# Performance work log

Measured on AMD Instinct MI355X. Metric: run time of the kernel, lower is better.

The kernel has to match this reference:

```python
import jax, jax.numpy as jnp
import numpy as np
from jax import lax

STRIDE = 2
PADDING = 2
KSIZE = 5


def _maxpool3d(y, k):
    # valid max pool with kernel=stride=k over the 3 spatial dims of NCDHW
    return lax.reduce_window(
        y, -jnp.inf, lax.max,
        window_dimensions=(1, 1, k, k, k),
        window_strides=(1, 1, k, k, k),
        padding='VALID')


def setup_inputs() -> dict:
    key = jax.random.key(0)
    k1, k2, k3 = jax.random.split(key, 3)
    x = jax.random.normal(k1, (16, 32, 16, 32, 32), dtype=jnp.float32)
    # torch ConvTranspose3d weight layout: (in_ch, out_ch, kD, kH, kW)
    weight = jax.random.normal(k2, (32, 64, KSIZE, KSIZE, KSIZE), dtype=jnp.float32) * 0.05
    bias = jax.random.normal(k3, (64,), dtype=jnp.float32) * 0.05
    return {"x": x, "weight": weight, "bias": bias}


def reference(x, weight, bias):
    # Fused ConvTranspose3d + sum over output channels.
    # sum_c convT(x, W)[:, c] == convT(x, W.sum(out_ch)) + bias.sum(), so we
    # pre-reduce the weight over the out-channel axis (axis=1) -- same math,
    # and it never materializes the (N, out_ch, D', H', W') intermediate,
    # exactly like the fused CUDA kernel.
    w_sum = weight.sum(axis=1)  # (in_ch, kD, kH, kW)
    # transposed conv == conv with lhs_dilation=stride, pad k-1-p, flipped kernel
    wk = w_sum[None, :, ::-1, ::-1, ::-1]  # (1, in_ch, kD, kH, kW), OIDHW
    pad = KSIZE - 1 - PADDING
    y = lax.conv_general_dilated(
        x, wk,
        window_strides=(1, 1, 1),
        padding=[(pad, pad)] * 3,
        lhs_dilation=(STRIDE, STRIDE, STRIDE),
        dimension_numbers=('NCDHW', 'OIDHW', 'NCDHW'))  # (N,1,31,63,63)
    y = y + bias.sum()
    # MaxPool3d(kernel=2) then MaxPool3d(kernel=3) on the single-channel map
    y = _maxpool3d(y, 2)  # (N,1,15,31,31)
    y = _maxpool3d(y, 3)  # (N,1,5,10,10)
    return y
```

## Files before the change

kernel.cpp:

```cpp
#include <hip/hip_runtime.h>


typedef short v8s __attribute__((ext_vector_type(8)));
typedef float v4f __attribute__((ext_vector_type(4)));
typedef unsigned short ushort_t;

#define CHSTR 16384
#define NSTRIDE (32*CHSTR)
#define Y_N 108000
#define Y_TOT (16*Y_N)
#define XSTR 24

#define XT_US 10653696u
#define XTN   665856u
#define PLANE_US 36992u
#define ROW_US 1088u
#define BT_BYTE_OFF 21307392u
#define WSF_BYTE_OFF 21335040u
#define NEED_MFMA (21335040u + 4097u*4u)

static __device__ __forceinline__ ushort_t f2bf(float f) {
  unsigned u = __builtin_bit_cast(unsigned, f);
  unsigned r = (u + 0x7FFFu + ((u >> 16) & 1u)) >> 16;
  return (ushort_t)r;
}

__global__ __launch_bounds__(256) void transpose_x(const float* __restrict__ x,
                                                   const float* __restrict__ w,
                                                   const float* __restrict__ bias,
                                                   ushort_t* __restrict__ xT,
                                                   ushort_t* __restrict__ Btab,
                                                   float* __restrict__ wsf) {
  int blk = blockIdx.x;
  int t = threadIdx.x;

  if (blk >= 1088) {
    int abc = blk - 1088;
    int a = abc / 9, b = (abc / 3) % 3, c = abc % 3;
    int half = t & 3;
    int l = t >> 2;
    int tt = l & 15, g = l >> 4;
    float v0 = 0.f, v1 = 0.f;
    if (tt < 8) {
      int td = tt & 1, th = (tt >> 1) & 1, tw = tt >> 2;
      int kd = td + 2 * a, kh = th + 2 * b, kw = tw + 2 * c;
      if (kd < 5 && kh < 5 && kw < 5) {
        int off = kd * 25 + kh * 5 + kw;
        const float* wp0 = w + (size_t)(8 * g + 2 * half) * 64 * 125 + off;
        const float* wp1 = wp0 + 64 * 125;
        float s0 = 0.f, s1 = 0.f;
#pragma unroll
        for (int oc = 0; oc < 64; ++oc) { s0 += wp0[oc * 125]; s1 += wp1[oc * 125]; }
        v0 = s0; v1 = s1;
      }
    }
    ((unsigned*)Btab)[(abc * 64 + l) * 4 + half] = (unsigned)f2bf(v0) | ((unsigned)f2bf(v1) << 16);
    if (abc == 0 && t == 0) {
      float bsum = 0.f;
      for (int o = 0; o < 64; ++o) bsum += bias[o];
      wsf[4096] = bsum;
    }
    return;
  }

  int hq = blk & 3;
  int dpad = (blk >> 2) % 17;
  int n = blk / 68;
  int h0 = 8 * hq;
  ushort_t* plane = xT + (size_t)(n * 18 + dpad) * PLANE_US;
  int d = dpad - 1;

  if (d < 0) {
    for (int r = 0; r < 8; ++r) {
      char* row = (char*)(plane + (size_t)(h0 + r) * ROW_US);
      for (int s = t; s < 136; s += 256)
        *(uint4*)(row + s * 16) = make_uint4(0, 0, 0, 0);
    }
    return;
  }

  __shared__ float lb[2][32 * 33];
  const float* xb = x + ((size_t)n * 32 * 16 + d) * 1024;
  int ic = t >> 3, wq = t & 7;

  {
    int h = h0 - 1;
    if (h >= 0) {
      float4 v = *(const float4*)&xb[(size_t)ic * 16384 + h * 32 + wq * 4];
      float* L = lb[0] + ic * 33 + wq * 4;
      L[0] = v.x; L[1] = v.y; L[2] = v.z; L[3] = v.w;
    }
  }
  int pp = 0;
  for (int i = 0; i < 8; ++i) {
    __syncthreads();
    if (i + 1 < 8) {
      int h = h0 + i;
      if (h <= 31) {
        float4 v = *(const float4*)&xb[(size_t)ic * 16384 + h * 32 + wq * 4];
        float* L = lb[pp ^ 1] + ic * 33 + wq * 4;
        L[0] = v.x; L[1] = v.y; L[2] = v.z; L[3] = v.w;
      }
    }
    int h = h0 + i - 1;
    ushort_t* row = plane + (size_t)(h0 + i) * ROW_US;
    bool hv = (h >= 0 && h <= 31);
    for (int s = t; s < 136; s += 256) {
      int wslot = s >> 2, q4 = s & 3;
      ushort_t o[8];
#pragma unroll
      for (int j = 0; j < 8; ++j) o[j] = 0;
      if (wslot >= 1 && wslot <= 32 && hv) {
        int w2 = wslot - 1;
        const float* L = lb[pp];
#pragma unroll
        for (int j = 0; j < 8; ++j) o[j] = f2bf(L[(8 * q4 + j) * 33 + w2]);
      }
      uint4 pk;
      pk.x = (unsigned)o[0] | ((unsigned)o[1] << 16);
      pk.y = (unsigned)o[2] | ((unsigned)o[3] << 16);
      pk.z = (unsigned)o[4] | ((unsigned)o[5] << 16);
      pk.w = (unsigned)o[6] | ((unsigned)o[7] << 16);
      *(uint4*)(row + wslot * 32 + q4 * 8) = pk;
    }
    pp ^= 1;
  }
}

__global__ __launch_bounds__(576, 7) void conv_mfma6(const ushort_t* __restrict__ xT,
                                                     const ushort_t* __restrict__ Btab,
                                                     const float* __restrict__ wsf,
                                                     float* __restrict__ out) {
  __shared__ __align__(16) char smem[35328];
  ushort_t* As0 = (ushort_t*)smem;
  ushort_t* As1 = (ushort_t*)(smem + 17408);
  float* ytile  = (float*)smem;
  float* red    = (float*)(smem + 34816);

  int blk = blockIdx.x;
  int OH2 = blk % 5, OD = (blk / 5) % 5, n = blk / 25;
  int t = threadIdx.x;
  int wv = t >> 6, l = t & 63;
  int mdl = wv / 3, mhp = wv % 3;
  int tt = l & 15, g = l >> 4;

  const ushort_t* xn = xT + (size_t)n * XTN;
  const ushort_t* slab0 = xn + ((size_t)(3 * OD) * 34 + 6 * OH2) * ROW_US;

  {
    uint4 v0 = *(const uint4*)(slab0 + (size_t)t * 8);
    uint4 v1;
    if (t < 512) v1 = *(const uint4*)(slab0 + (size_t)(t + 576) * 8);
    *(uint4*)&As0[t * 8] = v0;
    if (t < 512) *(uint4*)&As0[(t + 576) * 8] = v1;
  }
  __syncthreads();

  v4f acc[2][2];
#pragma unroll
  for (int m2 = 0; m2 < 2; ++m2)
#pragma unroll
    for (int wh = 0; wh < 2; ++wh) acc[m2][wh] = (v4f){0.f, 0.f, 0.f, 0.f};

  int lane_base = (2 * mhp) * ROW_US + tt * 32 + g * 8;

  for (int p = 0; p < 5; ++p) {
    uint4 v0, v1;
    if (p < 4) {
      const ushort_t* slab = slab0 + (size_t)(p + 1) * PLANE_US;
      v0 = *(const uint4*)(slab + (size_t)t * 8);
      if (t < 512) v1 = *(const uint4*)(slab + (size_t)(t + 576) * 8);
    }

    int a = mdl + 2 - p;
    if (0 <= a && a <= 2) {
      const ushort_t* Ab = (p & 1) ? As1 : As0;
      const ushort_t* Bg = Btab + ((size_t)(a * 9) * 64 + l) * 8;
#pragma unroll
      for (int c = 0; c < 3; ++c) {
        v8s bv0 = *(const v8s*)(Bg + (0 * 3 + c) * 512);
        v8s bv1 = *(const v8s*)(Bg + (1 * 3 + c) * 512);
        v8s bv2 = *(const v8s*)(Bg + (2 * 3 + c) * 512);
#pragma unroll
        for (int wh = 0; wh < 2; ++wh) {
          const ushort_t* ap = Ab + lane_base + (2 - c + 16 * wh) * 32;
          v8s a0 = *(const v8s*)(ap);
          v8s a1 = *(const v8s*)(ap + 1 * ROW_US);
          v8s a2 = *(const v8s*)(ap + 2 * ROW_US);
          v8s a3 = *(const v8s*)(ap + 3 * ROW_US);
          acc[0][wh] = __builtin_amdgcn_mfma_f32_16x16x32_bf16(a0, bv2, acc[0][wh], 0, 0, 0);
          acc[0][wh] = __builtin_amdgcn_mfma_f32_16x16x32_bf16(a1, bv1, acc[0][wh], 0, 0, 0);
          acc[0][wh] = __builtin_amdgcn_mfma_f32_16x16x32_bf16(a2, bv0, acc[0][wh], 0, 0, 0);
          acc[1][wh] = __builtin_amdgcn_mfma_f32_16x16x32_bf16(a1, bv2, acc[1][wh], 0, 0, 0);
          acc[1][wh] = __builtin_amdgcn_mfma_f32_16x16x32_bf16(a2, bv1, acc[1][wh], 0, 0, 0);
          acc[1][wh] = __builtin_amdgcn_mfma_f32_16x16x32_bf16(a3, bv0, acc[1][wh], 0, 0, 0);
        }
      }
    }

    if (p < 4) {
      ushort_t* dst = (p & 1) ? As0 : As1;
      *(uint4*)&dst[t * 8] = v0;
      if (t < 512) *(uint4*)&dst[(t + 576) * 8] = v1;
      __syncthreads();
    }
  }

  __syncthreads();
  if (tt < 8) {
    int td = tt & 1, th = (tt >> 1) & 1, tw = tt >> 2;
    int odl = 2 * mdl + td;
#pragma unroll
    for (int m2 = 0; m2 < 2; ++m2) {
      int ohl = 2 * (2 * mhp + m2) + th;
      float* yrow = &ytile[(odl * 12 + ohl) * 64];
#pragma unroll
      for (int wh = 0; wh < 2; ++wh)
#pragma unroll
        for (int i = 0; i < 4; ++i)
          yrow[2 * (16 * wh + 4 * g + i) + tw] = acc[m2][wh][i];
    }
  }
  __syncthreads();

  if (t < 120) {
    int OW = t % 10, p_oh = (t / 10) & 1, odl = t / 20;
    float m = -3.4e38f;
    for (int oh = 0; oh < 6; ++oh)
#pragma unroll
      for (int j = 0; j < 6; ++j)
        m = fmaxf(m, ytile[(odl * 12 + 6 * p_oh + oh) * 64 + 6 * OW + j]);
    red[t] = m;
  }
  __syncthreads();
  if (t < 20) {
    int OW = t % 10, p_oh = t / 10;
    float m = red[p_oh * 10 + OW];
#pragma unroll
    for (int odl = 1; odl < 6; ++odl) m = fmaxf(m, red[odl * 20 + p_oh * 10 + OW]);
    out[((n * 5 + OD) * 10 + (2 * OH2 + p_oh)) * 10 + OW] = m + wsf[4096];
  }
}

__global__ __launch_bounds__(128) void prep2(const float* __restrict__ w,
                                             const float* __restrict__ bias,
                                             float* __restrict__ ws, int woff) {
  int i = blockIdx.x, t = threadIdx.x;
  if (t < 125) {
    const float* wp = w + (size_t)i * 64 * 125 + t;
    float v = 0.f;
#pragma unroll
    for (int o = 0; o < 64; ++o) v += wp[o * 125];
    ws[woff + i * 128 + t] = v;
  }
  if (i == 0 && t == 126) {
    float b = 0.f;
    for (int o = 0; o < 64; ++o) b += bias[o];
    ws[woff + 4096] = b;
  }
}

__global__ __launch_bounds__(256, 4) void conv_stage1(const float* __restrict__ x,
                                                      const float* __restrict__ ws,
                                                      float* part, int woff) {
  __shared__ __align__(16) float xs[170 * XSTR];
  int blk = blockIdx.x;
  int s0 = blk % 320;
  int wq = s0 & 1, hq = (s0 >> 1) & 1, dc = (s0 >> 2) % 5, n = s0 / 20;
  int t = threadIdx.x;
  int mw = t % 15, lmh = t / 15;
  int id_base = 3 * dc - 1, ih_base = 15 * hq - 1;
  int iwb = wq ? 12 : -4;
  int cb = mw + (wq ? 2 : 3);
  const float* xn = x + (size_t)n * NSTRIDE;
  const float* wsw = ws + woff;
  float acc[3][2][2][2] = {{{{0.f}}}};
  for (int phs = 0; phs < 16; ++phs) {
    for (int s = t; s < 1700; s += 256) {
      int c2 = s % 10, row = s / 10;
      int bh = row % 17, q = row / 17;
      int ad = q % 5, lic = q / 5;
      int id = id_base + ad, ih = ih_base + bh, iw = iwb + 2 * c2;
      float2 v = make_float2(0.f, 0.f);
      if ((id | ih | iw) >= 0)
        v = *(const float2*)&xn[(size_t)(phs * 2 + lic) * CHSTR + (id * 32 + ih) * 32 + iw];
      *(float2*)&xs[row * XSTR + 2 * c2] = v;
    }
    __syncthreads();
    if (t < 225) {
#pragma unroll
      for (int lic = 0; lic < 2; ++lic) {
        const float* wc = wsw + (size_t)(phs * 2 + lic) * 128;
        const float* xc = &xs[(lic * 85 + lmh) * XSTR + cb];
        float xv[5][3][3];
#pragma unroll
        for (int a = 0; a < 5; ++a)
#pragma unroll
          for (int b = 0; b < 3; ++b) {
            const float* xr = xc + (a * 17 + b) * XSTR;
            xv[a][b][0] = xr[0]; xv[a][b][1] = xr[1]; xv[a][b][2] = xr[2];
          }
#pragma unroll
        for (int kd = 0; kd < 5; ++kd) {
          constexpr int DT[5] = {0, 1, 0, 1, 0};
          constexpr int AOFF[5] = {2, 2, 1, 1, 0};
          const int dt = DT[kd], aoff = AOFF[kd];
          float wvv[25];
#pragma unroll
          for (int j = 0; j < 25; ++j) wvv[j] = wc[kd * 25 + j];
#pragma unroll
          for (int kh = 0; kh < 5; ++kh) {
            constexpr int HT[5] = {0, 1, 0, 1, 0};
            constexpr int BOFF[5] = {2, 2, 1, 1, 0};
            const int ht = HT[kh], boff = BOFF[kh];
#pragma unroll
            for (int m = 0; m < 3; ++m) {
              const float x0 = xv[m + aoff][boff][0];
              const float x1 = xv[m + aoff][boff][1];
              const float x2 = xv[m + aoff][boff][2];
              acc[m][dt][ht][0] += x0 * wvv[kh * 5 + 4];
              acc[m][dt][ht][0] += x1 * wvv[kh * 5 + 2];
              acc[m][dt][ht][0] += x2 * wvv[kh * 5 + 0];
              acc[m][dt][ht][1] += x1 * wvv[kh * 5 + 3];
              acc[m][dt][ht][1] += x2 * wvv[kh * 5 + 1];
            }
          }
        }
      }
    }
    __syncthreads();
  }
  if (t < 225) {
    float* pb = part + (size_t)n * Y_N;
#pragma unroll
    for (int m = 0; m < 3; ++m)
#pragma unroll
      for (int dt = 0; dt < 2; ++dt)
#pragma unroll
        for (int ht = 0; ht < 2; ++ht) {
          int od_g = 6 * dc + 2 * m + dt;
          int oh_g = 30 * hq + 2 * lmh + ht;
          int ow_g = 30 * wq + 2 * mw;
          *(float2*)&pb[(od_g * 60 + oh_g) * 60 + ow_g] =
              make_float2(acc[m][dt][ht][0], acc[m][dt][ht][1]);
        }
  }
}

__global__ __launch_bounds__(256) void pool_stage2(const float* __restrict__ part,
                                                   const float* __restrict__ ws,
                                                   float* __restrict__ out, int woff) {
  __shared__ __align__(16) float buf[2160];
  __shared__ float red[240];
  int blk = blockIdx.x;
  int hc = blk % 10, dc = (blk / 10) % 5, n = blk / 50;
  int t = threadIdx.x;
  const float* pb = part + (size_t)n * Y_N;
  for (int s = t; s < 540; s += 256) {
    int row = s / 15, c4 = s % 15;
    int od = row / 6, oh = row % 6;
    size_t idx = (size_t)((6 * dc + od) * 60 + (6 * hc + oh)) * 60 + 4 * c4;
    *(float4*)&buf[row * 60 + 4 * c4] = *(const float4*)&pb[idx];
  }
  __syncthreads();
  if (t < 240) {
    int wc = t / 24, sub = t % 24;
    float m = -3.4e38f;
#pragma unroll
    for (int k = 0; k < 9; ++k) {
      int e = sub + 24 * k;
      int od = e / 36, r = e % 36;
      int oh = r / 6, ow0 = r % 6;
      m = fmaxf(m, buf[(od * 6 + oh) * 60 + 6 * wc + ow0]);
    }
    red[t] = m;
  }
  __syncthreads();
  if (t < 10) {
    float mm = -3.4e38f;
#pragma unroll
    for (int s2 = 0; s2 < 24; ++s2) mm = fmaxf(mm, red[t * 24 + s2]);
    out[((n * 5 + dc) * 10 + hc) * 10 + t] = mm + ws[woff + 4096];
  }
}

extern "C" void kernel_launch(void* const* d_in, const int* in_sizes, int n_in,
                              void* d_out, int out_size, void* d_ws, size_t ws_size,
                              hipStream_t stream) {
  const float* x    = (const float*)d_in[0];
  const float* w    = (const float*)d_in[1];
  const float* bias = (const float*)d_in[2];
  float* outp = (float*)d_out;

  if (ws_size >= (size_t)NEED_MFMA) {
    ushort_t* xT = (ushort_t*)d_ws;
    ushort_t* Bt = (ushort_t*)((char*)d_ws + BT_BYTE_OFF);
    float* wsf   = (float*)((char*)d_ws + WSF_BYTE_OFF);
    transpose_x<<<1088 + 27, 256, 0, stream>>>(x, w, bias, xT, Bt, wsf);
    conv_mfma6<<<400, 576, 0, stream>>>(xT, Bt, wsf, outp);
    return;
  }

  float* ws = (float*)d_ws;
  const size_t need1 = ((size_t)1 * Y_TOT + 4097) * 4;
  if (ws_size >= need1) {
    int woff = Y_TOT;
    prep2<<<32, 128, 0, stream>>>(w, bias, ws, woff);
    conv_stage1<<<320, 256, 0, stream>>>(x, ws, ws, woff);
    pool_stage2<<<800, 256, 0, stream>>>(ws, ws, outp, woff);
  }
}
```

Baseline: 36.05 us.

## Fuse x transpose and bf16 conversion into the MFMA conv kernel

Removes the separate transpose_x pass that wrote a padded bf16 channels-last copy of x to workspace. The conv kernel now reads fp32 x directly, converts it to bf16 and packs it into LDS, masking the halo rows and planes. It also remaps block indices so batch items spread across XCDs. This saves a full global round trip for x at the cost of strided, less coalesced loads in the conv kernel and a lower occupancy hint (5 instead of 7).

```diff
diff --git a/kernel.cpp b/kernel.cpp
--- a/kernel.cpp
+++ b/kernel.cpp
@@ -10,127 +10,56 @@
 #define Y_N 108000
 #define Y_TOT (16*Y_N)
 #define XSTR 24
-
-#define XT_US 10653696u
-#define XTN   665856u
-#define PLANE_US 36992u
-#define ROW_US 1088u
-#define BT_BYTE_OFF 21307392u
-#define WSF_BYTE_OFF 21335040u
-#define NEED_MFMA (21335040u + 4097u*4u)
+#define ROW_US 1088
+
+#define WSF_BYTE_OFF 27648u
+#define NEED_FUSED (27648u + 4097u*4u)
 
 static __device__ __forceinline__ ushort_t f2bf(float f) {
   unsigned u = __builtin_bit_cast(unsigned, f);
   unsigned r = (u + 0x7FFFu + ((u >> 16) & 1u)) >> 16;
   return (ushort_t)r;
 }
-
-__global__ __launch_bounds__(256) void transpose_x(const float* __restrict__ x,
-                                                   const float* __restrict__ w,
-                                                   const float* __restrict__ bias,
-                                                   ushort_t* __restrict__ xT,
-                                                   ushort_t* __restrict__ Btab,
-                                                   float* __restrict__ wsf) {
-  int blk = blockIdx.x;
+static __device__ __forceinline__ unsigned pk2(float a, float b) {
+  return (unsigned)f2bf(a) | ((unsigned)f2bf(b) << 16);
+}
+
+__global__ __launch_bounds__(256) void prep_bw(const float* __restrict__ w,
+                                               const float* __restrict__ bias,
+                                               ushort_t* __restrict__ Btab,
+                                               float* __restrict__ wsf) {
+  int abc = blockIdx.x;
+  int a = abc / 9, b = (abc / 3) % 3, c = abc % 3;
   int t = threadIdx.x;
-
-  if (blk >= 1088) {
-    int abc = blk - 1088;
-    int a = abc / 9, b = (abc / 3) % 3, c = abc % 3;
-    int half = t & 3;
-    int l = t >> 2;
-    int tt = l & 15, g = l >> 4;
-    float v0 = 0.f, v1 = 0.f;
-    if (tt < 8) {
-      int td = tt & 1, th = (tt >> 1) & 1, tw = tt >> 2;
-      int kd = td + 2 * a, kh = th + 2 * b, kw = tw + 2 * c;
-      if (kd < 5 && kh < 5 && kw < 5) {
-        int off = kd * 25 + kh * 5 + kw;
-        const float* wp0 = w + (size_t)(8 * g + 2 * half) * 64 * 125 + off;
-        const float* wp1 = wp0 + 64 * 125;
-        float s0 = 0.f, s1 = 0.f;
-#pragma unroll
-        for (int oc = 0; oc < 64; ++oc) { s0 += wp0[oc * 125]; s1 += wp1[oc * 125]; }
-        v0 = s0; v1 = s1;
-      }
-    }
-    ((unsigned*)Btab)[(abc * 64 + l) * 4 + half] = (unsigned)f2bf(v0) | ((unsigned)f2bf(v1) << 16);
-    if (abc == 0 && t == 0) {
-      float bsum = 0.f;
-      for (int o = 0; o < 64; ++o) bsum += bias[o];
-      wsf[4096] = bsum;
-    }
-    return;
-  }
-
-  int hq = blk & 3;
-  int dpad = (blk >> 2) % 17;
-  int n = blk / 68;
-  int h0 = 8 * hq;
-  ushort_t* plane = xT + (size_t)(n * 18 + dpad) * PLANE_US;
-  int d = dpad - 1;
-
-  if (d < 0) {
-    for (int r = 0; r < 8; ++r) {
-      char* row = (char*)(plane + (size_t)(h0 + r) * ROW_US);
-      for (int s = t; s < 136; s += 256)
-        *(uint4*)(row + s * 16) = make_uint4(0, 0, 0, 0);
-    }
-    return;
-  }
-
-  __shared__ float lb[2][32 * 33];
-  const float* xb = x + ((size_t)n * 32 * 16 + d) * 1024;
-  int ic = t >> 3, wq = t & 7;
-
-  {
-    int h = h0 - 1;
-    if (h >= 0) {
-      float4 v = *(const float4*)&xb[(size_t)ic * 16384 + h * 32 + wq * 4];
-      float* L = lb[0] + ic * 33 + wq * 4;
-      L[0] = v.x; L[1] = v.y; L[2] = v.z; L[3] = v.w;
-    }
-  }
-  int pp = 0;
-  for (int i = 0; i < 8; ++i) {
-    __syncthreads();
-    if (i + 1 < 8) {
-      int h = h0 + i;
-      if (h <= 31) {
-        float4 v = *(const float4*)&xb[(size_t)ic * 16384 + h * 32 + wq * 4];
-        float* L = lb[pp ^ 1] + ic * 33 + wq * 4;
-        L[0] = v.x; L[1] = v.y; L[2] = v.z; L[3] = v.w;
-      }
-    }
-    int h = h0 + i - 1;
-    ushort_t* row = plane + (size_t)(h0 + i) * ROW_US;
-    bool hv = (h >= 0 && h <= 31);
-    for (int s = t; s < 136; s += 256) {
-      int wslot = s >> 2, q4 = s & 3;
-      ushort_t o[8];
-#pragma unroll
-      for (int j = 0; j < 8; ++j) o[j] = 0;
-      if (wslot >= 1 && wslot <= 32 && hv) {
-        int w2 = wslot - 1;
-        const float* L = lb[pp];
-#pragma unroll
-        for (int j = 0; j < 8; ++j) o[j] = f2bf(L[(8 * q4 + j) * 33 + w2]);
-      }
-      uint4 pk;
-      pk.x = (unsigned)o[0] | ((unsigned)o[1] << 16);
-      pk.y = (unsigned)o[2] | ((unsigned)o[3] << 16);
-      pk.z = (unsigned)o[4] | ((unsigned)o[5] << 16);
-      pk.w = (unsigned)o[6] | ((unsigned)o[7] << 16);
-      *(uint4*)(row + wslot * 32 + q4 * 8) = pk;
-    }
-    pp ^= 1;
-  }
-}
-
-__global__ __launch_bounds__(576, 7) void conv_mfma6(const ushort_t* __restrict__ xT,
-                                                     const ushort_t* __restrict__ Btab,
-                                                     const float* __restrict__ wsf,
-                                                     float* __restrict__ out) {
+  int half = t & 3;
+  int l = t >> 2;
+  int tt = l & 15, g = l >> 4;
+  float v0 = 0.f, v1 = 0.f;
+  if (tt < 8) {
+    int td = tt & 1, th = (tt >> 1) & 1, tw = tt >> 2;
+    int kd = td + 2 * a, kh = th + 2 * b, kw = tw + 2 * c;
+    if (kd < 5 && kh < 5 && kw < 5) {
+      int off = kd * 25 + kh * 5 + kw;
+      const float* wp0 = w + (size_t)(8 * g + 2 * half) * 64 * 125 + off;
+      const float* wp1 = wp0 + 64 * 125;
+      float s0 = 0.f, s1 = 0.f;
+#pragma unroll
+      for (int oc = 0; oc < 64; ++oc) { s0 += wp0[oc * 125]; s1 += wp1[oc * 125]; }
+      v0 = s0; v1 = s1;
+    }
+  }
+  ((unsigned*)Btab)[(abc * 64 + l) * 4 + half] = (unsigned)f2bf(v0) | ((unsigned)f2bf(v1) << 16);
+  if (abc == 0 && t == 0) {
+    float bs = 0.f;
+    for (int o = 0; o < 64; ++o) bs += bias[o];
+    wsf[4096] = bs;
+  }
+}
+
+__global__ __launch_bounds__(576, 5) void conv_direct(const float* __restrict__ x,
+                                                      const ushort_t* __restrict__ Btab,
+                                                      const float* __restrict__ wsf,
+                                                      float* __restrict__ out) {
   __shared__ __align__(16) char smem[35328];
   ushort_t* As0 = (ushort_t*)smem;
   ushort_t* As1 = (ushort_t*)(smem + 17408);
@@ -138,21 +67,51 @@
   float* red    = (float*)(smem + 34816);
 
   int blk = blockIdx.x;
-  int OH2 = blk % 5, OD = (blk / 5) % 5, n = blk / 25;
+  int xcd = blk & 7;
+  int q = blk >> 3;
+  int n = xcd + 8 * (q / 25);
+  int cell = q % 25;
+  int OD = cell / 5, OH2 = cell % 5;
+
   int t = threadIdx.x;
   int wv = t >> 6, l = t & 63;
   int mdl = wv / 3, mhp = wv % 3;
   int tt = l & 15, g = l >> 4;
 
-  const ushort_t* xn = xT + (size_t)n * XTN;
-  const ushort_t* slab0 = xn + ((size_t)(3 * OD) * 34 + 6 * OH2) * ROW_US;
+  int r1 = t >> 7, w1g = (t >> 2) & 31, ich1 = t & 3;
+  int h1 = 6 * OH2 + r1 - 1;
+  float msk1 = (h1 >= 0) ? 1.f : 0.f;
+  const float* xb1 = x + (size_t)(n * 32 + ich1 * 8) * CHSTR + (h1 > 0 ? h1 : 0) * 32 + w1g;
+  int lds1 = (r1 * 34 + w1g + 1) * 32 + ich1 * 8;
+  bool has2 = (wv < 7);
+  int u2 = t + 576;
+  int r2 = u2 >> 7, w2g = (u2 >> 2) & 31, ich2 = u2 & 3;
+  int h2 = 6 * OH2 + r2 - 1;
+  const float* xb2 = x + (size_t)(n * 32 + ich2 * 8) * CHSTR + h2 * 32 + w2g;
+  int lds2 = (r2 * 34 + w2g + 1) * 32 + ich2 * 8;
+
+#define LOADU(F, P, DOFF) _Pragma("unroll") \
+  for (int j = 0; j < 8; ++j) F[j] = (P)[(size_t)j * CHSTR + (DOFF)];
+#define PACKW(DST, OFF, F, M) { uint4 _pk; \
+  _pk.x = pk2(F[0] * (M), F[1] * (M)); _pk.y = pk2(F[2] * (M), F[3] * (M)); \
+  _pk.z = pk2(F[4] * (M), F[5] * (M)); _pk.w = pk2(F[6] * (M), F[7] * (M)); \
+  *(uint4*)&(DST)[OFF] = _pk; }
 
   {
-    uint4 v0 = *(const uint4*)(slab0 + (size_t)t * 8);
-    uint4 v1;
-    if (t < 512) v1 = *(const uint4*)(slab0 + (size_t)(t + 576) * 8);
-    *(uint4*)&As0[t * 8] = v0;
-    if (t < 512) *(uint4*)&As0[(t + 576) * 8] = v1;
+    int d0 = 3 * OD - 1;
+    int doff = (d0 > 0 ? d0 : 0) * 1024;
+    float m0 = (d0 >= 0) ? 1.f : 0.f;
+    float f1[8], f2[8];
+    LOADU(f1, xb1, doff);
+    if (has2) LOADU(f2, xb2, doff);
+    PACKW(As0, lds1, f1, msk1 * m0);
+    if (has2) PACKW(As0, lds2, f2, m0);
+    if (t < 128) {
+      int bsel = t >> 6, idx = t & 63;
+      int rr = idx >> 3, side = (idx >> 2) & 1, qq = idx & 3;
+      ushort_t* B = bsel ? As1 : As0;
+      *(uint4*)&B[(rr * 34 + (side ? 33 : 0)) * 32 + qq * 8] = make_uint4(0, 0, 0, 0);
+    }
   }
   __syncthreads();
 
@@ -165,11 +124,11 @@
   int lane_base = (2 * mhp) * ROW_US + tt * 32 + g * 8;
 
   for (int p = 0; p < 5; ++p) {
-    uint4 v0, v1;
+    float pf1[8], pf2[8];
     if (p < 4) {
-      const ushort_t* slab = slab0 + (size_t)(p + 1) * PLANE_US;
-      v0 = *(const uint4*)(slab + (size_t)t * 8);
-      if (t < 512) v1 = *(const uint4*)(slab + (size_t)(t + 576) * 8);
+      int doff = (3 * OD + p) * 1024;
+      LOADU(pf1, xb1, doff);
+      if (has2) LOADU(pf2, xb2, doff);
     }
 
     int a = mdl + 2 - p;
@@ -200,8 +159,8 @@
 
     if (p < 4) {
       ushort_t* dst = (p & 1) ? As0 : As1;
-      *(uint4*)&dst[t * 8] = v0;
-      if (t < 512) *(uint4*)&dst[(t + 576) * 8] = v1;
+      PACKW(dst, lds1, pf1, msk1);
+      if (has2) PACKW(dst, lds2, pf2, 1.f);
       __syncthreads();
     }
   }
@@ -392,12 +351,11 @@
   const float* bias = (const float*)d_in[2];
   float* outp = (float*)d_out;
 
-  if (ws_size >= (size_t)NEED_MFMA) {
-    ushort_t* xT = (ushort_t*)d_ws;
-    ushort_t* Bt = (ushort_t*)((char*)d_ws + BT_BYTE_OFF);
+  if (ws_size >= (size_t)NEED_FUSED) {
+    ushort_t* Bt = (ushort_t*)d_ws;
     float* wsf   = (float*)((char*)d_ws + WSF_BYTE_OFF);
-    transpose_x<<<1088 + 27, 256, 0, stream>>>(x, w, bias, xT, Bt, wsf);
-    conv_mfma6<<<400, 576, 0, stream>>>(xT, Bt, wsf, outp);
+    prep_bw<<<27, 256, 0, stream>>>(w, bias, Bt, wsf);
+    conv_direct<<<400, 576, 0, stream>>>(x, Bt, wsf, outp);
     return;
   }
 
```

New measurement: 40.14 us. 1.11x slower.

## Fuse transpose/weight-prep and MFMA conv into one persistent kernel with atomic counters

Applied to the files above, without the earlier changes.

Merges the bf16 transpose/weight-reduction kernel and the MFMA conv kernel into a single 400-block launch. Each block first does up to three transpose or prep work units, then bumps per-batch atomic counters, and spins until its batch's 68 planes and all 27 weight tiles are ready. The aim is to remove the second kernel launch and the gap between the two kernels, and to let conv blocks start as soon as their own batch is transposed. In exchange it adds a memset launch, spin-wait latency, and lower parallelism in the transpose phase (576-thread blocks with only 256 active). It also relies on all 400 blocks being co-resident to avoid deadlock.

```diff
diff --git a/kernel.cpp b/kernel.cpp
--- a/kernel.cpp
+++ b/kernel.cpp
@@ -11,13 +11,13 @@
 #define Y_TOT (16*Y_N)
 #define XSTR 24
 
-#define XT_US 10653696u
 #define XTN   665856u
 #define PLANE_US 36992u
 #define ROW_US 1088u
 #define BT_BYTE_OFF 21307392u
 #define WSF_BYTE_OFF 21335040u
-#define NEED_MFMA (21335040u + 4097u*4u)
+#define CNT_BYTE_OFF 21351488u
+#define NEED_FUSED (21351488u + 128u)
 
 static __device__ __forceinline__ ushort_t f2bf(float f) {
   unsigned u = __builtin_bit_cast(unsigned, f);
@@ -25,121 +25,146 @@
   return (ushort_t)r;
 }
 
-__global__ __launch_bounds__(256) void transpose_x(const float* __restrict__ x,
-                                                   const float* __restrict__ w,
-                                                   const float* __restrict__ bias,
-                                                   ushort_t* __restrict__ xT,
-                                                   ushort_t* __restrict__ Btab,
-                                                   float* __restrict__ wsf) {
-  int blk = blockIdx.x;
-  int t = threadIdx.x;
-
-  if (blk >= 1088) {
-    int abc = blk - 1088;
-    int a = abc / 9, b = (abc / 3) % 3, c = abc % 3;
-    int half = t & 3;
-    int l = t >> 2;
-    int tt = l & 15, g = l >> 4;
-    float v0 = 0.f, v1 = 0.f;
-    if (tt < 8) {
-      int td = tt & 1, th = (tt >> 1) & 1, tw = tt >> 2;
-      int kd = td + 2 * a, kh = th + 2 * b, kw = tw + 2 * c;
-      if (kd < 5 && kh < 5 && kw < 5) {
-        int off = kd * 25 + kh * 5 + kw;
-        const float* wp0 = w + (size_t)(8 * g + 2 * half) * 64 * 125 + off;
-        const float* wp1 = wp0 + 64 * 125;
-        float s0 = 0.f, s1 = 0.f;
-#pragma unroll
-        for (int oc = 0; oc < 64; ++oc) { s0 += wp0[oc * 125]; s1 += wp1[oc * 125]; }
-        v0 = s0; v1 = s1;
-      }
-    }
-    ((unsigned*)Btab)[(abc * 64 + l) * 4 + half] = (unsigned)f2bf(v0) | ((unsigned)f2bf(v1) << 16);
-    if (abc == 0 && t == 0) {
-      float bsum = 0.f;
-      for (int o = 0; o < 64; ++o) bsum += bias[o];
-      wsf[4096] = bsum;
-    }
-    return;
-  }
-
-  int hq = blk & 3;
-  int dpad = (blk >> 2) % 17;
-  int n = blk / 68;
-  int h0 = 8 * hq;
-  ushort_t* plane = xT + (size_t)(n * 18 + dpad) * PLANE_US;
-  int d = dpad - 1;
-
-  if (d < 0) {
-    for (int r = 0; r < 8; ++r) {
-      char* row = (char*)(plane + (size_t)(h0 + r) * ROW_US);
-      for (int s = t; s < 136; s += 256)
-        *(uint4*)(row + s * 16) = make_uint4(0, 0, 0, 0);
-    }
-    return;
-  }
-
-  __shared__ float lb[2][32 * 33];
-  const float* xb = x + ((size_t)n * 32 * 16 + d) * 1024;
-  int ic = t >> 3, wq = t & 7;
-
-  {
-    int h = h0 - 1;
-    if (h >= 0) {
-      float4 v = *(const float4*)&xb[(size_t)ic * 16384 + h * 32 + wq * 4];
-      float* L = lb[0] + ic * 33 + wq * 4;
-      L[0] = v.x; L[1] = v.y; L[2] = v.z; L[3] = v.w;
-    }
-  }
-  int pp = 0;
-  for (int i = 0; i < 8; ++i) {
+__global__ __launch_bounds__(576, 7) void fused_all(const float* __restrict__ x,
+                                                    const float* __restrict__ wt,
+                                                    const float* __restrict__ bias,
+                                                    ushort_t* __restrict__ xT,
+                                                    ushort_t* __restrict__ Btab,
+                                                    float* __restrict__ wsf,
+                                                    unsigned* __restrict__ cnt,
+                                                    float* __restrict__ out) {
+  __shared__ __align__(16) char smem[35328];
+  int b = blockIdx.x, t = threadIdx.x;
+
+  float* lb = (float*)smem;
+  for (int k = 0; k < 3; ++k) {
+    int u;
+    bool isprep = false;
+    if (k == 0) {
+      if (b < 373) u = b; else { isprep = true; u = b - 373; }
+    } else if (k == 1) {
+      u = 373 + b;
+    } else {
+      u = 773 + b;
+      if (u >= 1088) break;
+    }
+
+    if (isprep) {
+      if (t < 256) {
+        int abc = u;
+        int a = abc / 9, bb = (abc / 3) % 3, c = abc % 3;
+        int half = t & 3;
+        int l = t >> 2;
+        int tt = l & 15, g = l >> 4;
+        float v0 = 0.f, v1 = 0.f;
+        if (tt < 8) {
+          int td = tt & 1, th = (tt >> 1) & 1, tw = tt >> 2;
+          int kd = td + 2 * a, kh = th + 2 * bb, kw = tw + 2 * c;
+          if (kd < 5 && kh < 5 && kw < 5) {
+            int off = kd * 25 + kh * 5 + kw;
+            const float* wp0 = wt + (size_t)(8 * g + 2 * half) * 64 * 125 + off;
+            const float* wp1 = wp0 + 64 * 125;
+            float s0 = 0.f, s1 = 0.f;
+#pragma unroll
+            for (int oc = 0; oc < 64; ++oc) { s0 += wp0[oc * 125]; s1 += wp1[oc * 125]; }
+            v0 = s0; v1 = s1;
+          }
+        }
+        ((unsigned*)Btab)[(abc * 64 + l) * 4 + half] =
+            (unsigned)f2bf(v0) | ((unsigned)f2bf(v1) << 16);
+        if (abc == 0 && t == 0) {
+          float bs = 0.f;
+          for (int o = 0; o < 64; ++o) bs += bias[o];
+          wsf[4096] = bs;
+        }
+      }
+      __syncthreads();
+      if (t == 0)
+        __hip_atomic_fetch_add(&cnt[16], 1u, __ATOMIC_RELEASE, __HIP_MEMORY_SCOPE_AGENT);
+      continue;
+    }
+
+    int hq = u & 3, dpad = (u >> 2) % 17, tn = u / 68;
+    int h0 = 8 * hq;
+    ushort_t* plane = xT + (size_t)(tn * 18 + dpad) * PLANE_US;
+    int d = dpad - 1;
+
+    if (d < 0) {
+      if (t < 256) {
+        for (int r = 0; r < 8; ++r) {
+          char* row = (char*)(plane + (size_t)(h0 + r) * ROW_US);
+          for (int s = t; s < 136; s += 256)
+            *(uint4*)(row + s * 16) = make_uint4(0, 0, 0, 0);
+        }
+      }
+    } else {
+      const float* xb = x + ((size_t)tn * 32 * 16 + d) * 1024;
+      int ic = t >> 3, wq = t & 7;
+      if (t < 256) {
+        int h = h0 - 1;
+        if (h >= 0) {
+          float4 v = *(const float4*)&xb[(size_t)ic * 16384 + h * 32 + wq * 4];
+          float* L = lb + ic * 33 + wq * 4;
+          L[0] = v.x; L[1] = v.y; L[2] = v.z; L[3] = v.w;
+        }
+      }
+      int pp = 0;
+      for (int i = 0; i < 8; ++i) {
+        __syncthreads();
+        if (t < 256) {
+          if (i + 1 < 8) {
+            int h = h0 + i;
+            if (h <= 31) {
+              float4 v = *(const float4*)&xb[(size_t)ic * 16384 + h * 32 + wq * 4];
+              float* L = lb + (pp ^ 1) * 1056 + ic * 33 + wq * 4;
+              L[0] = v.x; L[1] = v.y; L[2] = v.z; L[3] = v.w;
+            }
+          }
+          int h = h0 + i - 1;
+          ushort_t* row = plane + (size_t)(h0 + i) * ROW_US;
+          bool hv = (h >= 0 && h <= 31);
+          const float* L = lb + pp * 1056;
+          for (int s = t; s < 136; s += 256) {
+            int wslot = s >> 2, q4 = s & 3;
+            ushort_t o[8];
+#pragma unroll
+            for (int j = 0; j < 8; ++j) o[j] = 0;
+            if (wslot >= 1 && wslot <= 32 && hv) {
+              int w2 = wslot - 1;
+#pragma unroll
+              for (int j = 0; j < 8; ++j) o[j] = f2bf(L[(8 * q4 + j) * 33 + w2]);
+            }
+            uint4 pk;
+            pk.x = (unsigned)o[0] | ((unsigned)o[1] << 16);
+            pk.y = (unsigned)o[2] | ((unsigned)o[3] << 16);
+            pk.z = (unsigned)o[4] | ((unsigned)o[5] << 16);
+            pk.w = (unsigned)o[6] | ((unsigned)o[7] << 16);
+            *(uint4*)(row + wslot * 32 + q4 * 8) = pk;
+          }
+        }
+        pp ^= 1;
+      }
+    }
     __syncthreads();
-    if (i + 1 < 8) {
-      int h = h0 + i;
-      if (h <= 31) {
-        float4 v = *(const float4*)&xb[(size_t)ic * 16384 + h * 32 + wq * 4];
-        float* L = lb[pp ^ 1] + ic * 33 + wq * 4;
-        L[0] = v.x; L[1] = v.y; L[2] = v.z; L[3] = v.w;
-      }
-    }
-    int h = h0 + i - 1;
-    ushort_t* row = plane + (size_t)(h0 + i) * ROW_US;
-    bool hv = (h >= 0 && h <= 31);
-    for (int s = t; s < 136; s += 256) {
-      int wslot = s >> 2, q4 = s & 3;
-      ushort_t o[8];
-#pragma unroll
-      for (int j = 0; j < 8; ++j) o[j] = 0;
-      if (wslot >= 1 && wslot <= 32 && hv) {
-        int w2 = wslot - 1;
-        const float* L = lb[pp];
-#pragma unroll
-        for (int j = 0; j < 8; ++j) o[j] = f2bf(L[(8 * q4 + j) * 33 + w2]);
-      }
-      uint4 pk;
-      pk.x = (unsigned)o[0] | ((unsigned)o[1] << 16);
-      pk.y = (unsigned)o[2] | ((unsigned)o[3] << 16);
-      pk.z = (unsigned)o[4] | ((unsigned)o[5] << 16);
-      pk.w = (unsigned)o[6] | ((unsigned)o[7] << 16);
-      *(uint4*)(row + wslot * 32 + q4 * 8) = pk;
-    }
-    pp ^= 1;
-  }
-}
-
-__global__ __launch_bounds__(576, 7) void conv_mfma6(const ushort_t* __restrict__ xT,
-                                                     const ushort_t* __restrict__ Btab,
-                                                     const float* __restrict__ wsf,
-                                                     float* __restrict__ out) {
-  __shared__ __align__(16) char smem[35328];
+    if (t == 0)
+      __hip_atomic_fetch_add(&cnt[tn], 1u, __ATOMIC_RELEASE, __HIP_MEMORY_SCOPE_AGENT);
+  }
+
+  int OH2 = b % 5, OD = (b / 5) % 5, n = b / 25;
+  if (t == 0) {
+    while (__hip_atomic_load(&cnt[16], __ATOMIC_RELAXED, __HIP_MEMORY_SCOPE_AGENT) < 27u)
+      __builtin_amdgcn_s_sleep(16);
+    while (__hip_atomic_load(&cnt[n], __ATOMIC_RELAXED, __HIP_MEMORY_SCOPE_AGENT) < 68u)
+      __builtin_amdgcn_s_sleep(16);
+  }
+  __syncthreads();
+  __builtin_amdgcn_fence(__ATOMIC_ACQUIRE, "agent");
+
   ushort_t* As0 = (ushort_t*)smem;
   ushort_t* As1 = (ushort_t*)(smem + 17408);
   float* ytile  = (float*)smem;
   float* red    = (float*)(smem + 34816);
 
-  int blk = blockIdx.x;
-  int OH2 = blk % 5, OD = (blk / 5) % 5, n = blk / 25;
-  int t = threadIdx.x;
   int wv = t >> 6, l = t & 63;
   int mdl = wv / 3, mhp = wv % 3;
   int tt = l & 15, g = l >> 4;
@@ -392,12 +417,13 @@
   const float* bias = (const float*)d_in[2];
   float* outp = (float*)d_out;
 
-  if (ws_size >= (size_t)NEED_MFMA) {
+  if (ws_size >= (size_t)NEED_FUSED) {
     ushort_t* xT = (ushort_t*)d_ws;
     ushort_t* Bt = (ushort_t*)((char*)d_ws + BT_BYTE_OFF);
     float* wsf   = (float*)((char*)d_ws + WSF_BYTE_OFF);
-    transpose_x<<<1088 + 27, 256, 0, stream>>>(x, w, bias, xT, Bt, wsf);
-    conv_mfma6<<<400, 576, 0, stream>>>(xT, Bt, wsf, outp);
+    unsigned* cnt = (unsigned*)((char*)d_ws + CNT_BYTE_OFF);
+    hipMemsetAsync(cnt, 0, 128, stream);
+    fused_all<<<400, 576, 0, stream>>>(x, w, bias, xT, Bt, wsf, cnt, outp);
     return;
   }
 
```

Result: slower. 111.6 us (+209.7%).
